# Kernel optimization log

Hardware: AMD Instinct MI355X
Metric: run time of the kernel (lower is better)

## Reference

```python
import jax, jax.numpy as jnp
import numpy as np

C_CURV = 1.0      # manifold curvature c (= k in the torch code)
EPS = 1e-15
PROJ_EPS = 1e-5   # standard Poincare ball boundary eps for manifold.proj


def _clamp_abs(x, eps=EPS):
    return jnp.maximum(jnp.abs(x), eps) * jnp.sign(x)


def setup_inputs() -> dict:
    key = jax.random.key(0)
    k1, k2, k3 = jax.random.split(key, 3)
    B, D, C = 4096, 1024, 4096
    c = C_CURV
    x = jax.random.normal(k1, (B, D), dtype=jnp.float32)
    # reset_parameters(): a ~ N(0, D^-0.5 / sqrt(c)); p ~ N(0, 0.1) clipped to norm 0.9/sqrt(c)
    a = jax.random.normal(k2, (C, D), dtype=jnp.float32) * (D ** -0.5 / c ** 0.5)
    p = jax.random.normal(k3, (C, D), dtype=jnp.float32) * 0.1
    p_norm = jnp.linalg.norm(p, axis=1, keepdims=True)
    max_norm = 0.9 / jnp.sqrt(jnp.float32(c))
    p = p * jnp.minimum(max_norm / p_norm, 1.0)
    return {"x": x, "a": a, "p": p}


def _forward(x, a, p):
    k = jnp.float32(C_CURV)
    sqrt_k = jnp.sqrt(k)

    # manifold.proj: clip x to the open ball of radius (1 - eps)/sqrt(c)
    xn = jnp.maximum(jnp.linalg.norm(x, axis=-1, keepdims=True), EPS)
    maxn = (1.0 - PROJ_EPS) / sqrt_k
    x = jnp.where(xn > maxn, x * (maxn / xn), x)

    # Rank-structured Mobius addition: diff = mobius_add(-p, x) factors as
    #   diff[b,c,:] = (A[b,c] * (-p[c]) + Bc[c] * x[b]) / den[b,c]
    x2 = jnp.sum(x * x, axis=-1)          # [B]
    p2 = jnp.sum(p * p, axis=-1)          # [C]
    px = jnp.einsum('bd,cd->bc', x, p)    # [B,C]  <p_c, x_b>
    xa = jnp.einsum('bd,cd->bc', x, a)    # [B,C]  <a_c, x_b>
    pa = jnp.sum(p * a, axis=-1)          # [C]    <p_c, a_c>
    a_norm = jnp.sqrt(jnp.sum(a * a, axis=-1))  # [C]

    A = 1.0 - 2.0 * k * px + k * x2[:, None]                       # [B,C]
    Bc = 1.0 - k * p2                                              # [C]
    den = jnp.maximum(1.0 - 2.0 * k * px + (k * k) * x2[:, None] * p2[None, :], EPS)

    diff_norm2 = jnp.maximum(
        (A * A * p2[None, :] + (Bc * Bc)[None, :] * x2[:, None] - 2.0 * A * Bc[None, :] * px)
        / (den * den), EPS)                                        # [B,C]
    sc_diff_a = (-A * pa[None, :] + Bc[None, :] * xa) / den        # [B,C], signed

    num = 2.0 * sc_diff_a
    denom = _clamp_abs((1.0 + k * diff_norm2) * a_norm[None, :])
    distance = jnp.arcsinh(sqrt_k * num / denom) / sqrt_k
    return -distance  # logits [B,C]


def reference(x, a, p):
    return _forward(x, a, p)
```

## Files before the change

kernel.cpp:

```cpp
#include <hip/hip_runtime.h>
#include <hip/hip_bf16.h>
#include <math.h>


#define EPSF 1e-15f
#define MAXN 0.99999f

constexpr int Bdim = 4096;
constexpr int Ddim = 1024;
constexpr int Cdim = 4096;

typedef __bf16 bf16x8 __attribute__((ext_vector_type(8)));
typedef float  f32x4  __attribute__((ext_vector_type(4)));
typedef unsigned short u16;

__device__ __forceinline__ u16 f2bf(float f) {
  __hip_bfloat16 h = __float2bfloat16(f);
  return *reinterpret_cast<const u16*>(&h);
}

__device__ __forceinline__ void gl_lds16(const u16* g, u16* l) {
  __builtin_amdgcn_global_load_lds(
      (const __attribute__((address_space(1))) void*)g,
      (__attribute__((address_space(3))) void*)l, 16, 0, 0);
}


__global__ __launch_bounds__(256) void prep_x(const float* __restrict__ x,
                                              u16* __restrict__ xb,
                                              float* __restrict__ x2o) {
  const int b = blockIdx.x, t = threadIdx.x;
  float4 v = ((const float4*)(x + (size_t)b * Ddim))[t];
  float s = v.x * v.x + v.y * v.y + v.z * v.z + v.w * v.w;
  __shared__ float red[4];
#pragma unroll
  for (int o = 32; o > 0; o >>= 1) s += __shfl_down(s, o);
  if ((t & 63) == 0) red[t >> 6] = s;
  __syncthreads();
  s = red[0] + red[1] + red[2] + red[3];
  float norm  = sqrtf(s);
  float xn    = fmaxf(norm, EPSF);
  float scale = (xn > MAXN) ? (MAXN / xn) : 1.0f;
  if (t == 0) x2o[b] = s * scale * scale;
  ushort4 o4;
  o4.x = f2bf(v.x * scale); o4.y = f2bf(v.y * scale);
  o4.z = f2bf(v.z * scale); o4.w = f2bf(v.w * scale);
  ((ushort4*)(xb + (size_t)b * Ddim))[t] = o4;
}

__global__ __launch_bounds__(256) void prep_pa(const float* __restrict__ a,
                                               const float* __restrict__ p,
                                               u16* __restrict__ pab,
                                               float* __restrict__ p2o,
                                               float* __restrict__ pao,
                                               float* __restrict__ ano) {
  const int c = blockIdx.x, t = threadIdx.x;
  float4 av = ((const float4*)(a + (size_t)c * Ddim))[t];
  float4 pv = ((const float4*)(p + (size_t)c * Ddim))[t];
  float sp2 = pv.x * pv.x + pv.y * pv.y + pv.z * pv.z + pv.w * pv.w;
  float spa = pv.x * av.x + pv.y * av.y + pv.z * av.z + pv.w * av.w;
  float sa2 = av.x * av.x + av.y * av.y + av.z * av.z + av.w * av.w;
  __shared__ float red[12];
#pragma unroll
  for (int o = 32; o > 0; o >>= 1) {
    sp2 += __shfl_down(sp2, o);
    spa += __shfl_down(spa, o);
    sa2 += __shfl_down(sa2, o);
  }
  if ((t & 63) == 0) { int w = t >> 6; red[w] = sp2; red[4 + w] = spa; red[8 + w] = sa2; }
  __syncthreads();
  if (t == 0) {
    p2o[c] = red[0] + red[1] + red[2] + red[3];
    pao[c] = red[4] + red[5] + red[6] + red[7];
    ano[c] = sqrtf(red[8] + red[9] + red[10] + red[11]);
  }
  const int prP = ((c >> 4) << 5) + (c & 15);
  ushort4 oa, op;
  oa.x = f2bf(av.x); oa.y = f2bf(av.y); oa.z = f2bf(av.z); oa.w = f2bf(av.w);
  op.x = f2bf(pv.x); op.y = f2bf(pv.y); op.z = f2bf(pv.z); op.w = f2bf(pv.w);
  ((ushort4*)(pab + (size_t)prP * Ddim))[t]        = op;
  ((ushort4*)(pab + (size_t)(prP + 16) * Ddim))[t] = oa;
}


#define LGKM_BAR() do {                                          \
    asm volatile("s_waitcnt lgkmcnt(0)" ::: "memory");           \
    __builtin_amdgcn_s_barrier();                                \
    __builtin_amdgcn_sched_barrier(0);                           \
  } while (0)

__global__ __launch_bounds__(512, 2) void gemm_ep(
    const u16* __restrict__ xb, const u16* __restrict__ pab,
    const float* __restrict__ x2g, const float* __restrict__ p2g,
    const float* __restrict__ pag, const float* __restrict__ ang,
    float* __restrict__ out) {
  __shared__ u16 Xs[2][2][8192];
  __shared__ u16 PAs[2][2][8192];

  const int t = threadIdx.x;

  const int flat  = blockIdx.y * 32 + blockIdx.x;
  const int swz   = (flat & 7) * 64 + (flat >> 3);
  const int chunk = swz >> 6;
  const int local = swz & 63;
  const int bx = chunk * 4 + (local & 3);
  const int by = local >> 2;

  const int lane = t & 63;
  const int wid  = t >> 6;
  const int wr   = wid >> 2;
  const int wc   = wid & 3;

  const int r0  = t >> 2;
  const int sw8 = ((t & 3) ^ ((r0 >> 1) & 3)) * 8;
  const u16* xsrc  = xb  + (size_t)(by * 256 + r0) * Ddim + sw8;
  const u16* pasrc = pab + (size_t)(bx * 256 + r0) * Ddim + sw8;
  const int t8 = t * 8;
  const size_t half = (size_t)128 * Ddim;

  const int arow = wr * 128 + (lane & 15);
  const int brow = wc * 64  + (lane & 15);
  const int aoff = arow * 32 + (((lane >> 4) ^ ((arow >> 1) & 3)) * 8);
  const int boff = brow * 32 + (((lane >> 4) ^ ((brow >> 1) & 3)) * 8);

  f32x4 acc[8][4];
  const f32x4 zero = {0.f, 0.f, 0.f, 0.f};
#pragma unroll
  for (int m = 0; m < 8; ++m)
#pragma unroll
    for (int n = 0; n < 4; ++n) acc[m][n] = zero;

  bf16x8 bv[4];

#define LOADBV(PR, XB) do {                                      \
    _Pragma("unroll")                                            \
    for (int nf = 0; nf < 4; ++nf)                               \
      bv[nf] = *(const bf16x8*)&(PR)[(XB) + boff + nf * 512];    \
  } while (0)

#define QUAD(XR, ABASE, XB) do {                                 \
    bf16x8 a0 = *(const bf16x8*)&(XR)[(XB) + aoff];              \
    bf16x8 a1 = *(const bf16x8*)&(XR)[(XB) + aoff + 512];        \
    bf16x8 a2 = *(const bf16x8*)&(XR)[(XB) + aoff + 1024];       \
    bf16x8 a3 = *(const bf16x8*)&(XR)[(XB) + aoff + 1536];       \
    __builtin_amdgcn_s_setprio(1);                               \
    _Pragma("unroll")                                            \
    for (int nf = 0; nf < 4; ++nf) {                             \
      acc[(ABASE)+0][nf] = __builtin_amdgcn_mfma_f32_16x16x32_bf16(a0, bv[nf], acc[(ABASE)+0][nf], 0, 0, 0); \
      acc[(ABASE)+1][nf] = __builtin_amdgcn_mfma_f32_16x16x32_bf16(a1, bv[nf], acc[(ABASE)+1][nf], 0, 0, 0); \
      acc[(ABASE)+2][nf] = __builtin_amdgcn_mfma_f32_16x16x32_bf16(a2, bv[nf], acc[(ABASE)+2][nf], 0, 0, 0); \
      acc[(ABASE)+3][nf] = __builtin_amdgcn_mfma_f32_16x16x32_bf16(a3, bv[nf], acc[(ABASE)+3][nf], 0, 0, 0); \
    }                                                            \
    __builtin_amdgcn_s_setprio(0);                               \
  } while (0)

  const u16* xgp = xsrc  + 64;
  const u16* pgp = pasrc + 64;

  {
    u16* Xw  = (u16*)&Xs[0][0][0];
    u16* PAw = (u16*)&PAs[0][0][0];
    gl_lds16(xsrc,             Xw + t8);
    gl_lds16(xsrc + half,      Xw + 4096 + t8);
    gl_lds16(pasrc,            PAw + t8);
    gl_lds16(pasrc + half,     PAw + 4096 + t8);
    gl_lds16(xsrc + 32,        Xw + 8192 + t8);
    gl_lds16(xsrc + half + 32, Xw + 8192 + 4096 + t8);
    gl_lds16(pasrc + 32,       PAw + 8192 + t8);
    gl_lds16(pasrc + half + 32,PAw + 8192 + 4096 + t8);
  }
  asm volatile("s_waitcnt vmcnt(4)" ::: "memory");
  __builtin_amdgcn_s_barrier();
  __builtin_amdgcn_sched_barrier(0);

  for (int T = 0; T < 15; ++T) {
    const int b = T & 1;
    const u16* Xr  = &Xs[b][0][0];
    const u16* PAr = &PAs[b][0][0];
    u16* Xw  = (u16*)&Xs[b ^ 1][0][0];
    u16* PAw = (u16*)&PAs[b ^ 1][0][0];

    gl_lds16(xgp,        Xw + t8);
    gl_lds16(xgp + half, Xw + 4096 + t8);
    LOADBV(PAr, 0);
    QUAD(Xr, 0, 0);
    LGKM_BAR();

    gl_lds16(pgp,        PAw + t8);
    gl_lds16(pgp + half, PAw + 4096 + t8);
    QUAD(Xr, 4, 2048);
    asm volatile("s_waitcnt vmcnt(4)" ::: "memory");
    LGKM_BAR();

    gl_lds16(xgp + 32,        Xw + 8192 + t8);
    gl_lds16(xgp + half + 32, Xw + 8192 + 4096 + t8);
    LOADBV(PAr, 8192);
    QUAD(Xr, 0, 8192);
    LGKM_BAR();

    gl_lds16(pgp + 32,        PAw + 8192 + t8);
    gl_lds16(pgp + half + 32, PAw + 8192 + 4096 + t8);
    QUAD(Xr, 4, 8192 + 2048);
    xgp += 64; pgp += 64;
    asm volatile("s_waitcnt vmcnt(4)" ::: "memory");
    LGKM_BAR();
  }

  {
    const u16* Xr  = &Xs[1][0][0];
    const u16* PAr = &PAs[1][0][0];
    LOADBV(PAr, 0);
    QUAD(Xr, 0, 0);
    LGKM_BAR();
    QUAD(Xr, 4, 2048);
    asm volatile("s_waitcnt vmcnt(0)" ::: "memory");
    LGKM_BAR();
    LOADBV(PAr, 8192);
    QUAD(Xr, 0, 8192);
    LGKM_BAR();
    QUAD(Xr, 4, 8192 + 2048);
  }

#undef LOADBV
#undef QUAD

#pragma unroll
  for (int m = 0; m < 8; ++m) {
    const int rl0 = by * 256 + wr * 128 + m * 16 + (lane >> 4) * 4;
    float x2r[4];
#pragma unroll
    for (int j = 0; j < 4; ++j) x2r[j] = x2g[rl0 + j];
#pragma unroll
    for (int g = 0; g < 2; ++g) {
      const int cl = (bx * 8 + wc * 2 + g) * 16 + (lane & 15);
      const float p2c = p2g[cl];
      const float pac = pag[cl];
      const float anc = ang[cl];
      const float Bcc = 1.0f - p2c;
      f32x4 px4 = acc[m][2 * g];
      f32x4 xa4 = acc[m][2 * g + 1];
#pragma unroll
      for (int j = 0; j < 4; ++j) {
        const float px = px4[j];
        const float xa = xa4[j];
        const float Av  = 1.0f - 2.0f * px + x2r[j];
        const float den = fmaxf(1.0f - 2.0f * px + x2r[j] * p2c, EPSF);
        const float dn2 = fmaxf((Av * Av * p2c + Bcc * Bcc * x2r[j] - 2.0f * Av * Bcc * px) / (den * den), EPSF);
        const float sc  = (Bcc * xa - Av * pac) / den;
        const float dv  = fmaxf((1.0f + dn2) * anc, EPSF);
        const float z   = (2.0f * sc) / dv;
        const float z2 = z * z;
        float r;
        if (z2 > 0.04f) r = asinhf(z);
        else            r = z * (1.0f - z2 * (1.0f / 6.0f) + z2 * z2 * 0.075f);
        out[(size_t)rl0 * Cdim + j * Cdim + cl] = -r;
      }
    }
  }
}

extern "C" void kernel_launch(void* const* d_in, const int* in_sizes, int n_in,
                              void* d_out, int out_size, void* d_ws, size_t ws_size,
                              hipStream_t stream) {
  const float* x = (const float*)d_in[0];
  const float* a = (const float*)d_in[1];
  const float* p = (const float*)d_in[2];
  float* out = (float*)d_out;

  char* ws = (char*)d_ws;
  u16* xb  = (u16*)(ws);
  u16* pab = (u16*)(ws + (size_t)8 * 1024 * 1024);
  float* x2 = (float*)(ws + (size_t)24 * 1024 * 1024);
  float* p2 = x2 + Bdim;
  float* pa = p2 + Cdim;
  float* an = pa + Cdim;

  prep_x <<<Bdim, 256, 0, stream>>>(x, xb, x2);
  prep_pa<<<Cdim, 256, 0, stream>>>(a, p, pab, p2, pa, an);
  gemm_ep<<<dim3(32, 16), 512, 0, stream>>>(xb, pab, x2, p2, pa, an, out);
}
```

Measured before the change: 125.5 us.

## Restructure GEMM main loop into issue-loads, barrier, MFMA, barrier phases

Splits each quarter-step into an LDS read phase and a separate MFMA phase. All A and B fragment reads and the async global-to-LDS copies are issued first, followed by a barrier and an lgkmcnt wait, then the MFMA block and a closing barrier. The aim is an 8-wave ping-pong style schedule where waves alternate between memory issue and matrix-core work, so LDS latency is not exposed inside the MFMA chains. It doubles the number of barriers per iteration and holds the A fragments in extra live registers, which may raise VGPR pressure under the 512x2 launch bound.

After: 129.2 us. 2.9% more time.

```diff
diff --git a/kernel.cpp b/kernel.cpp
--- a/kernel.cpp
+++ b/kernel.cpp
@@ -83,11 +83,19 @@
 }
 
 
-#define LGKM_BAR() do {                                          \
+#define BAR_LGKM() do {                                          \
+    __builtin_amdgcn_s_barrier();                                \
     asm volatile("s_waitcnt lgkmcnt(0)" ::: "memory");           \
+    __builtin_amdgcn_sched_barrier(0);                           \
+  } while (0)
+
+#define ENDBAR() do {                                            \
     __builtin_amdgcn_s_barrier();                                \
     __builtin_amdgcn_sched_barrier(0);                           \
   } while (0)
+
+#define GATE4() asm volatile("s_waitcnt vmcnt(4)" ::: "memory")
+#define GATE0() asm volatile("s_waitcnt vmcnt(0)" ::: "memory")
 
 __global__ __launch_bounds__(512, 2) void gemm_ep(
     const u16* __restrict__ xb, const u16* __restrict__ pab,
@@ -131,6 +139,7 @@
     for (int n = 0; n < 4; ++n) acc[m][n] = zero;
 
   bf16x8 bv[4];
+  bf16x8 av0, av1, av2, av3;
 
 #define LOADBV(PR, XB) do {                                      \
     _Pragma("unroll")                                            \
@@ -138,18 +147,21 @@
       bv[nf] = *(const bf16x8*)&(PR)[(XB) + boff + nf * 512];    \
   } while (0)
 
-#define QUAD(XR, ABASE, XB) do {                                 \
-    bf16x8 a0 = *(const bf16x8*)&(XR)[(XB) + aoff];              \
-    bf16x8 a1 = *(const bf16x8*)&(XR)[(XB) + aoff + 512];        \
-    bf16x8 a2 = *(const bf16x8*)&(XR)[(XB) + aoff + 1024];       \
-    bf16x8 a3 = *(const bf16x8*)&(XR)[(XB) + aoff + 1536];       \
+#define LOADA(XR, XB) do {                                       \
+    av0 = *(const bf16x8*)&(XR)[(XB) + aoff];                    \
+    av1 = *(const bf16x8*)&(XR)[(XB) + aoff + 512];              \
+    av2 = *(const bf16x8*)&(XR)[(XB) + aoff + 1024];             \
+    av3 = *(const bf16x8*)&(XR)[(XB) + aoff + 1536];             \
+  } while (0)
+
+#define MFMA16(ABASE) do {                                       \
     __builtin_amdgcn_s_setprio(1);                               \
     _Pragma("unroll")                                            \
     for (int nf = 0; nf < 4; ++nf) {                             \
-      acc[(ABASE)+0][nf] = __builtin_amdgcn_mfma_f32_16x16x32_bf16(a0, bv[nf], acc[(ABASE)+0][nf], 0, 0, 0); \
-      acc[(ABASE)+1][nf] = __builtin_amdgcn_mfma_f32_16x16x32_bf16(a1, bv[nf], acc[(ABASE)+1][nf], 0, 0, 0); \
-      acc[(ABASE)+2][nf] = __builtin_amdgcn_mfma_f32_16x16x32_bf16(a2, bv[nf], acc[(ABASE)+2][nf], 0, 0, 0); \
-      acc[(ABASE)+3][nf] = __builtin_amdgcn_mfma_f32_16x16x32_bf16(a3, bv[nf], acc[(ABASE)+3][nf], 0, 0, 0); \
+      acc[(ABASE)+0][nf] = __builtin_amdgcn_mfma_f32_16x16x32_bf16(av0, bv[nf], acc[(ABASE)+0][nf], 0, 0, 0); \
+      acc[(ABASE)+1][nf] = __builtin_amdgcn_mfma_f32_16x16x32_bf16(av1, bv[nf], acc[(ABASE)+1][nf], 0, 0, 0); \
+      acc[(ABASE)+2][nf] = __builtin_amdgcn_mfma_f32_16x16x32_bf16(av2, bv[nf], acc[(ABASE)+2][nf], 0, 0, 0); \
+      acc[(ABASE)+3][nf] = __builtin_amdgcn_mfma_f32_16x16x32_bf16(av3, bv[nf], acc[(ABASE)+3][nf], 0, 0, 0); \
     }                                                            \
     __builtin_amdgcn_s_setprio(0);                               \
   } while (0)
@@ -169,7 +181,7 @@
     gl_lds16(pasrc + 32,       PAw + 8192 + t8);
     gl_lds16(pasrc + half + 32,PAw + 8192 + 4096 + t8);
   }
-  asm volatile("s_waitcnt vmcnt(4)" ::: "memory");
+  GATE4();
   __builtin_amdgcn_s_barrier();
   __builtin_amdgcn_sched_barrier(0);
 
@@ -180,49 +192,69 @@
     u16* Xw  = (u16*)&Xs[b ^ 1][0][0];
     u16* PAw = (u16*)&PAs[b ^ 1][0][0];
 
+    LOADBV(PAr, 0);
+    LOADA(Xr, 0);
     gl_lds16(xgp,        Xw + t8);
     gl_lds16(xgp + half, Xw + 4096 + t8);
-    LOADBV(PAr, 0);
-    QUAD(Xr, 0, 0);
-    LGKM_BAR();
-
+    BAR_LGKM();
+    MFMA16(0);
+    ENDBAR();
+
+    LOADA(Xr, 2048);
     gl_lds16(pgp,        PAw + t8);
     gl_lds16(pgp + half, PAw + 4096 + t8);
-    QUAD(Xr, 4, 2048);
-    asm volatile("s_waitcnt vmcnt(4)" ::: "memory");
-    LGKM_BAR();
-
+    BAR_LGKM();
+    MFMA16(4);
+    GATE4();
+    ENDBAR();
+
+    LOADBV(PAr, 8192);
+    LOADA(Xr, 8192);
     gl_lds16(xgp + 32,        Xw + 8192 + t8);
     gl_lds16(xgp + half + 32, Xw + 8192 + 4096 + t8);
-    LOADBV(PAr, 8192);
-    QUAD(Xr, 0, 8192);
-    LGKM_BAR();
-
+    BAR_LGKM();
+    MFMA16(0);
+    ENDBAR();
+
+    LOADA(Xr, 8192 + 2048);
     gl_lds16(pgp + 32,        PAw + 8192 + t8);
     gl_lds16(pgp + half + 32, PAw + 8192 + 4096 + t8);
-    QUAD(Xr, 4, 8192 + 2048);
+    BAR_LGKM();
+    MFMA16(4);
     xgp += 64; pgp += 64;
-    asm volatile("s_waitcnt vmcnt(4)" ::: "memory");
-    LGKM_BAR();
+    GATE4();
+    ENDBAR();
   }
 
   {
     const u16* Xr  = &Xs[1][0][0];
     const u16* PAr = &PAs[1][0][0];
     LOADBV(PAr, 0);
-    QUAD(Xr, 0, 0);
-    LGKM_BAR();
-    QUAD(Xr, 4, 2048);
-    asm volatile("s_waitcnt vmcnt(0)" ::: "memory");
-    LGKM_BAR();
+    LOADA(Xr, 0);
+    BAR_LGKM();
+    MFMA16(0);
+    ENDBAR();
+
+    LOADA(Xr, 2048);
+    BAR_LGKM();
+    MFMA16(4);
+    GATE0();
+    ENDBAR();
+
     LOADBV(PAr, 8192);
-    QUAD(Xr, 0, 8192);
-    LGKM_BAR();
-    QUAD(Xr, 4, 8192 + 2048);
+    LOADA(Xr, 8192);
+    BAR_LGKM();
+    MFMA16(0);
+    ENDBAR();
+
+    LOADA(Xr, 8192 + 2048);
+    BAR_LGKM();
+    MFMA16(4);
   }
 
 #undef LOADBV
-#undef QUAD
+#undef LOADA
+#undef MFMA16
 
 #pragma unroll
   for (int m = 0; m < 8; ++m) {
```
